# Kernel optimization log

Measured on AMD Instinct MI355X. Metric: run time of the kernel, lower is better.

## Reference

```python
import jax, jax.numpy as jnp
import numpy as np

N = 50000
E = 800000
NEG_SLOPE = 0.2
BN_EPS = 1e-5


def _gat_conv(x, src, dst, W, a_src, a_dst, bias, heads, out_ch, concat):
    # Linear projection per head: [N, heads, out_ch]
    h = (x @ W).reshape(-1, heads, out_ch)
    # Per-node attention terms alpha_src/alpha_dst: [N, heads]
    al_s = (h * a_src[None]).sum(-1)
    al_d = (h * a_dst[None]).sum(-1)
    # Edge logits with LeakyReLU: [E, heads]
    logits = jax.nn.leaky_relu(al_s[src] + al_d[dst], NEG_SLOPE)
    # Segment (scatter) softmax over edges grouped by destination node
    m = jax.ops.segment_max(logits, dst, num_segments=N)
    e = jnp.exp(logits - m[dst])
    s = jax.ops.segment_sum(e, dst, num_segments=N)
    alpha = e / (s[dst] + 1e-16)                      # [E, heads]
    # Weighted message aggregation: scatter-add to destinations
    msg = h[src] * alpha[:, :, None]                  # [E, heads, out_ch]
    out = jax.ops.segment_sum(msg, dst, num_segments=N)  # [N, heads, out_ch]
    out = out.reshape(-1, heads * out_ch) if concat else out.mean(axis=1)
    return out + bias


def _bn_eval(x, gamma, beta, mean, var):
    return (x - mean) * jax.lax.rsqrt(var + BN_EPS) * gamma + beta


def setup_inputs() -> dict:
    key = jax.random.key(0)
    ks = jax.random.split(key, 12)
    in_ch, hid, heads, out_cls = 128, 64, 2, 40
    return {
        "x": jax.random.normal(ks[0], (N, in_ch), jnp.float32),
        "edge_index": jax.random.randint(ks[1], (2, E), 0, N, jnp.int32),
        "W1": jax.random.normal(ks[2], (in_ch, heads * hid), jnp.float32) * 0.1,
        "a1_src": jax.random.normal(ks[3], (heads, hid), jnp.float32) * 0.1,
        "a1_dst": jax.random.normal(ks[4], (heads, hid), jnp.float32) * 0.1,
        "b1": jnp.zeros((heads * hid,), jnp.float32),
        "bn1_gamma": jnp.ones((heads * hid,), jnp.float32),
        "bn1_beta": jnp.zeros((heads * hid,), jnp.float32),
        "bn1_mean": jax.random.normal(ks[5], (heads * hid,), jnp.float32) * 0.1,
        "bn1_var": jax.random.uniform(ks[6], (heads * hid,), jnp.float32, 0.5, 1.5),
        "W2": jax.random.normal(ks[7], (heads * hid, out_cls), jnp.float32) * 0.1,
        "a2_src": jax.random.normal(ks[8], (1, out_cls), jnp.float32) * 0.1,
        "a2_dst": jax.random.normal(ks[9], (1, out_cls), jnp.float32) * 0.1,
        "b2": jnp.zeros((out_cls,), jnp.float32),
    }


def reference(x, edge_index, W1, a1_src, a1_dst, b1, bn1_gamma, bn1_beta,
              bn1_mean, bn1_var, W2, a2_src, a2_dst, b2):
    # add self loops
    loops = jnp.arange(N, dtype=edge_index.dtype)
    src = jnp.concatenate([edge_index[0], loops])
    dst = jnp.concatenate([edge_index[1], loops])
    # layer 1: GATConv(heads=2, concat) -> BN(eval) -> ReLU (dropout is eval no-op)
    h = _gat_conv(x, src, dst, W1, a1_src, a1_dst, b1, heads=2, out_ch=64, concat=True)
    h = jax.nn.relu(_bn_eval(h, bn1_gamma, bn1_beta, bn1_mean, bn1_var))
    # output layer: GATConv(heads=1, concat=False)
    out = _gat_conv(h, src, dst, W2, a2_src, a2_dst, b2, heads=1, out_ch=40, concat=False)
    return jax.nn.log_softmax(out, axis=1)
```

## Files before the change

### kernel.cpp

```cpp
#include <hip/hip_runtime.h>
#include <hip/hip_bf16.h>

#define NEG_SLOPE 0.2f
#define BN_EPS 1e-5f

#define NBLK 256
#define COARSE_SHIFT 9
#define COARSE_NPB 512

__device__ __forceinline__ float wred_sum(float v) {
    #pragma unroll
    for (int m = 32; m > 0; m >>= 1) v += __shfl_xor(v, m);
    return v;
}
__device__ __forceinline__ float wred_max(float v) {
    #pragma unroll
    for (int m = 32; m > 0; m >>= 1) v = fmaxf(v, __shfl_xor(v, m));
    return v;
}

__device__ __forceinline__ unsigned pack_bf16(float a, float b) {
    __hip_bfloat162 t;
    t.x = __float2bfloat16(a);
    t.y = __float2bfloat16(b);
    return *(unsigned*)&t;
}
__device__ __forceinline__ float2 unpack_bf16(unsigned u) {
    __hip_bfloat162 t = *(__hip_bfloat162*)&u;
    return {__bfloat162float(t.x), __bfloat162float(t.y)};
}

__device__ __forceinline__ unsigned enc_ord(float f) {
    unsigned u = __float_as_uint(f);
    return (u & 0x80000000u) ? ~u : (u | 0x80000000u);
}
__device__ __forceinline__ float dec_ord(unsigned e) {
    unsigned u = (e & 0x80000000u) ? (e ^ 0x80000000u) : ~e;
    return __uint_as_float(u);
}

__global__ __launch_bounds__(256) void part_hist(const int* __restrict__ ei, int E, int Et,
                                                 int chunk, int* __restrict__ hist, int nCoarse) {
    __shared__ int h[128];
    int b = blockIdx.x, t = threadIdx.x;
    if (t < 128) h[t] = 0;
    __syncthreads();
    int beg = b * chunk, end = min(beg + chunk, Et);
    for (int idx = beg + t; idx < end; idx += 256) {
        int d = (idx < E) ? ei[E + idx] : (idx - E);
        atomicAdd(&h[d >> COARSE_SHIFT], 1);
    }
    __syncthreads();
    if (t < nCoarse) hist[t * NBLK + b] = h[t];
}

__global__ __launch_bounds__(256) void coarse_total(const int* __restrict__ hist,
                                                    int* __restrict__ ctot) {
    __shared__ int red[256];
    int c = blockIdx.x, t = threadIdx.x;
    red[t] = hist[c * NBLK + t];
    __syncthreads();
    for (int off = 128; off > 0; off >>= 1) {
        if (t < off) red[t] += red[t + off];
        __syncthreads();
    }
    if (t == 0) ctot[c] = red[0];
}

__global__ __launch_bounds__(128) void coarse_scan(const int* __restrict__ ctot,
                                                   int* __restrict__ cbase, int nCoarse) {
    __shared__ int s[128];
    int t = threadIdx.x;
    int v = (t < nCoarse) ? ctot[t] : 0;
    s[t] = v;
    __syncthreads();
    for (int off = 1; off < 128; off <<= 1) {
        int u = (t >= off) ? s[t - off] : 0;
        __syncthreads();
        s[t] += u;
        __syncthreads();
    }
    if (t < nCoarse) cbase[t] = s[t] - v;
    if (t == 127) cbase[nCoarse] = s[127];
}

__global__ __launch_bounds__(64) void part_scan(int* __restrict__ hist,
                                                const int* __restrict__ cbase, int nCoarse) {
    int c = blockIdx.x, t = threadIdx.x;
    int base = cbase[c];
    int idx = c * NBLK + 4 * t;
    int4 v = *(int4*)&hist[idx];
    int sl = v.x + v.y + v.z + v.w;
    int inc = sl;
    #pragma unroll
    for (int off = 1; off < 64; off <<= 1) {
        int u = __shfl_up(inc, off);
        if (t >= off) inc += u;
    }
    int exc = inc - sl + base;
    int4 o;
    o.x = exc;
    o.y = exc + v.x;
    o.z = exc + v.x + v.y;
    o.w = exc + v.x + v.y + v.z;
    *(int4*)&hist[idx] = o;
}

__global__ __launch_bounds__(256) void part_scatter(const int* __restrict__ ei, int E, int Et,
                                                    int chunk, const int* __restrict__ hist,
                                                    unsigned* __restrict__ staged, int nCoarse) {
    __shared__ int cur[128];
    int b = blockIdx.x, t = threadIdx.x;
    if (t < nCoarse) cur[t] = hist[t * NBLK + b];
    __syncthreads();
    int beg = b * chunk, end = min(beg + chunk, Et);
    for (int idx = beg + t; idx < end; idx += 256) {
        int s, d;
        if (idx < E) { s = ei[idx]; d = ei[E + idx]; }
        else         { s = idx - E; d = idx - E; }
        int c = d >> COARSE_SHIFT;
        int pos = atomicAdd(&cur[c], 1);
        staged[pos] = ((unsigned)s << COARSE_SHIFT) | (unsigned)(d & (COARSE_NPB - 1));
    }
}

__global__ __launch_bounds__(512) void fine_place(const unsigned* __restrict__ staged,
                                                  const int* __restrict__ cbase,
                                                  int* __restrict__ offs,
                                                  int* __restrict__ csr, int Nn, int nCoarse) {
    __shared__ int hcnt[COARSE_NPB];
    __shared__ int scn[COARSE_NPB];
    int b = blockIdx.x, t = threadIdx.x;
    int node0 = b << COARSE_SHIFT;
    int nloc = min(COARSE_NPB, Nn - node0);
    hcnt[t] = 0;
    __syncthreads();
    int ebeg = cbase[b], eend = cbase[b + 1];
    for (int p = ebeg + t; p < eend; p += 512) {
        atomicAdd(&hcnt[staged[p] & (COARSE_NPB - 1)], 1);
    }
    __syncthreads();
    int val = hcnt[t];
    scn[t] = val;
    __syncthreads();
    for (int off = 1; off < COARSE_NPB; off <<= 1) {
        int u = (t >= off) ? scn[t - off] : 0;
        __syncthreads();
        scn[t] += u;
        __syncthreads();
    }
    int exc = ebeg + scn[t] - val;
    if (t < nloc) offs[node0 + t] = exc;
    if (b == nCoarse - 1 && t == 0) offs[Nn] = eend;
    hcnt[t] = exc;
    __syncthreads();
    for (int p = ebeg + t; p < eend; p += 512) {
        unsigned v = staged[p];
        int pos = atomicAdd(&hcnt[v & (COARSE_NPB - 1)], 1);
        csr[pos] = (int)(v >> COARSE_SHIFT);
    }
}

__global__ __launch_bounds__(256) void gemm1_tiled(const float* __restrict__ x,
                                                   const float* __restrict__ W,
                                                   const float* __restrict__ a1s,
                                                   const float* __restrict__ a1d,
                                                   unsigned* __restrict__ h1b,
                                                   float* __restrict__ als,
                                                   float* __restrict__ ald,
                                                   unsigned* __restrict__ gmax, int Nn) {
    __shared__ float As[64][33];
    __shared__ float Bs[32][132];
    __shared__ float4 red4[64][17];
    int t  = threadIdx.x;
    int tx = t & 15;
    int ty = t >> 4;
    int br = blockIdx.x * 64;

    float acc[4][8];
    #pragma unroll
    for (int i = 0; i < 4; ++i)
        #pragma unroll
        for (int j = 0; j < 8; ++j) acc[i][j] = 0.f;

    int k4  = t & 7;
    int rowA = t >> 3;

    for (int k0 = 0; k0 < 128; k0 += 32) {
        #pragma unroll
        for (int i = 0; i < 2; ++i) {
            int r  = rowA + 32 * i;
            int gr = min(br + r, Nn - 1);
            float4 v = *(const float4*)(x + (size_t)gr * 128 + k0 + 4 * k4);
            As[r][4 * k4 + 0] = v.x; As[r][4 * k4 + 1] = v.y;
            As[r][4 * k4 + 2] = v.z; As[r][4 * k4 + 3] = v.w;
        }
        #pragma unroll
        for (int i = 0; i < 4; ++i) {
            int f  = t + 256 * i;
            int kk = f >> 5, c4 = f & 31;
            *(float4*)&Bs[kk][4 * c4] = *(const float4*)(W + (size_t)(k0 + kk) * 128 + 4 * c4);
        }
        __syncthreads();
        #pragma unroll
        for (int kk = 0; kk < 32; ++kk) {
            float4 b0 = *(const float4*)&Bs[kk][4 * tx];
            float4 b1 = *(const float4*)&Bs[kk][64 + 4 * tx];
            #pragma unroll
            for (int i = 0; i < 4; ++i) {
                float a = As[4 * ty + i][kk];
                acc[i][0] += a * b0.x; acc[i][1] += a * b0.y;
                acc[i][2] += a * b0.z; acc[i][3] += a * b0.w;
                acc[i][4] += a * b1.x; acc[i][5] += a * b1.y;
                acc[i][6] += a * b1.z; acc[i][7] += a * b1.w;
            }
        }
        __syncthreads();
    }
    float s_lo[4], s_hi[4], d_lo[4], d_hi[4];
    #pragma unroll
    for (int j = 0; j < 4; ++j) {
        s_lo[j] = a1s[4 * tx + j];      s_hi[j] = a1s[64 + 4 * tx + j];
        d_lo[j] = a1d[4 * tx + j];      d_hi[j] = a1d[64 + 4 * tx + j];
    }
    #pragma unroll
    for (int i = 0; i < 4; ++i) {
        float4 pp = {0.f, 0.f, 0.f, 0.f};
        #pragma unroll
        for (int j = 0; j < 4; ++j) {
            pp.x += acc[i][j] * s_lo[j];
            pp.y += acc[i][4 + j] * s_hi[j];
            pp.z += acc[i][j] * d_lo[j];
            pp.w += acc[i][4 + j] * d_hi[j];
        }
        red4[4 * ty + i][tx] = pp;
        int r = br + 4 * ty + i;
        if (r < Nn) {
            uint2 lo = {pack_bf16(acc[i][0], acc[i][1]), pack_bf16(acc[i][2], acc[i][3])};
            uint2 hi = {pack_bf16(acc[i][4], acc[i][5]), pack_bf16(acc[i][6], acc[i][7])};
            *(uint2*)(h1b + (size_t)r * 64 + 2 * tx)      = lo;
            *(uint2*)(h1b + (size_t)r * 64 + 32 + 2 * tx) = hi;
        }
    }
    __syncthreads();
    if (t < 64) {
        int r = br + t;
        float4 s = {0.f, 0.f, 0.f, 0.f};
        #pragma unroll
        for (int xx = 0; xx < 16; ++xx) {
            float4 p = red4[t][xx];
            s.x += p.x; s.y += p.y; s.z += p.z; s.w += p.w;
        }
        if (r < Nn) {
            als[r * 2] = s.x; als[r * 2 + 1] = s.y;
            ald[r * 2] = s.z; ald[r * 2 + 1] = s.w;
        }
        float m0 = wred_max(s.x);
        float m1 = wred_max(s.y);
        if (t == 0) {
            atomicMax(&gmax[0], enc_ord(m0));
            atomicMax(&gmax[1], enc_ord(m1));
        }
    }
}

__global__ __launch_bounds__(256) void softagg1_kernel(const int* __restrict__ offs, const int* __restrict__ csr,
                            const unsigned* __restrict__ h1b,
                            const float* __restrict__ als, const float* __restrict__ ald,
                            const unsigned* __restrict__ gmax,
                            const float* __restrict__ b1, const float* __restrict__ gam,
                            const float* __restrict__ bet, const float* __restrict__ mean,
                            const float* __restrict__ var, float* __restrict__ hbn, int Nn) {
    int wid = threadIdx.x >> 6, lane = threadIdx.x & 63;
    int n = blockIdx.x * 4 + wid;
    if (n >= Nn) return;
    int b = offs[n], e = offs[n + 1];
    int sub = lane >> 4;
    int l16 = lane & 15;
    int head = l16 >> 3;
    float aldh = ald[n * 2 + head];
    float bound = dec_ord(gmax[head]) + aldh;
    bound = (bound > 0.f) ? bound : NEG_SLOPE * bound;

    float acc[8];
    #pragma unroll
    for (int j = 0; j < 8; ++j) acc[j] = 0.f;
    float den = 0.f;
    for (int p = b + sub; p < e; p += 4) {
        int s = csr[p];
        float al = als[s * 2 + head] + aldh;
        al = (al > 0.f) ? al : NEG_SLOPE * al;
        float ev = __expf(al - bound);
        uint4 v = *(const uint4*)(h1b + (size_t)s * 64 + 4 * l16);
        float2 f0 = unpack_bf16(v.x), f1 = unpack_bf16(v.y);
        float2 f2 = unpack_bf16(v.z), f3 = unpack_bf16(v.w);
        acc[0] += f0.x * ev; acc[1] += f0.y * ev;
        acc[2] += f1.x * ev; acc[3] += f1.y * ev;
        acc[4] += f2.x * ev; acc[5] += f2.y * ev;
        acc[6] += f3.x * ev; acc[7] += f3.y * ev;
        den += ev;
    }
    #pragma unroll
    for (int j = 0; j < 8; ++j) {
        acc[j] += __shfl_xor(acc[j], 16);
        acc[j] += __shfl_xor(acc[j], 32);
    }
    den += __shfl_xor(den, 16);
    den += __shfl_xor(den, 32);
    if (sub == 0) {
        float inv = 1.f / (den + 1e-16f);
        int c = 8 * l16;
        #pragma unroll
        for (int half = 0; half < 2; ++half) {
            int cc = c + 4 * half;
            float4 bb = *(const float4*)(b1 + cc);
            float4 gg = *(const float4*)(gam + cc);
            float4 be = *(const float4*)(bet + cc);
            float4 mm = *(const float4*)(mean + cc);
            float4 vv = *(const float4*)(var + cc);
            float4 o;
            o.x = fmaxf((acc[4*half+0] * inv + bb.x - mm.x) * rsqrtf(vv.x + BN_EPS) * gg.x + be.x, 0.f);
            o.y = fmaxf((acc[4*half+1] * inv + bb.y - mm.y) * rsqrtf(vv.y + BN_EPS) * gg.y + be.y, 0.f);
            o.z = fmaxf((acc[4*half+2] * inv + bb.z - mm.z) * rsqrtf(vv.z + BN_EPS) * gg.z + be.z, 0.f);
            o.w = fmaxf((acc[4*half+3] * inv + bb.w - mm.w) * rsqrtf(vv.w + BN_EPS) * gg.w + be.w, 0.f);
            *(float4*)(hbn + (size_t)n * 128 + cc) = o;
        }
    }
}

__global__ __launch_bounds__(256) void gemm2_tiled(const float* __restrict__ hbn,
                                                   const float* __restrict__ W2,
                                                   const float* __restrict__ a2s,
                                                   const float* __restrict__ a2d,
                                                   unsigned* __restrict__ h2b,
                                                   float* __restrict__ als, float* __restrict__ ald,
                                                   unsigned* __restrict__ gmax, int Nn) {
    __shared__ float As[64][33];
    __shared__ float Bs[128][68];
    __shared__ float redS[64][17];
    __shared__ float redD[64][17];
    int t  = threadIdx.x;
    int tx = t & 15;
    int ty = t >> 4;
    int br = blockIdx.x * 64;

    #pragma unroll
    for (int i = 0; i < 8; ++i) {
        int f  = t + 256 * i;
        int kk = f >> 4, c4 = f & 15;
        float4 v = {0.f, 0.f, 0.f, 0.f};
        if (c4 < 10) v = *(const float4*)(W2 + (size_t)kk * 40 + 4 * c4);
        *(float4*)&Bs[kk][4 * c4] = v;
    }
    float as4[4], ad4[4];
    #pragma unroll
    for (int j = 0; j < 4; ++j) {
        int c = 4 * tx + j;
        as4[j] = (c < 40) ? a2s[c] : 0.f;
        ad4[j] = (c < 40) ? a2d[c] : 0.f;
    }

    float acc[4][4];
    #pragma unroll
    for (int i = 0; i < 4; ++i)
        #pragma unroll
        for (int j = 0; j < 4; ++j) acc[i][j] = 0.f;

    int k4  = t & 7;
    int rowA = t >> 3;
    __syncthreads();

    for (int k0 = 0; k0 < 128; k0 += 32) {
        #pragma unroll
        for (int i = 0; i < 2; ++i) {
            int r  = rowA + 32 * i;
            int gr = min(br + r, Nn - 1);
            float4 v = *(const float4*)(hbn + (size_t)gr * 128 + k0 + 4 * k4);
            As[r][4 * k4 + 0] = v.x; As[r][4 * k4 + 1] = v.y;
            As[r][4 * k4 + 2] = v.z; As[r][4 * k4 + 3] = v.w;
        }
        __syncthreads();
        #pragma unroll
        for (int kk = 0; kk < 32; ++kk) {
            float4 b0 = *(const float4*)&Bs[k0 + kk][4 * tx];
            #pragma unroll
            for (int i = 0; i < 4; ++i) {
                float a = As[4 * ty + i][kk];
                acc[i][0] += a * b0.x; acc[i][1] += a * b0.y;
                acc[i][2] += a * b0.z; acc[i][3] += a * b0.w;
            }
        }
        __syncthreads();
    }
    #pragma unroll
    for (int i = 0; i < 4; ++i) {
        redS[4 * ty + i][tx] = acc[i][0] * as4[0] + acc[i][1] * as4[1] + acc[i][2] * as4[2] + acc[i][3] * as4[3];
        redD[4 * ty + i][tx] = acc[i][0] * ad4[0] + acc[i][1] * ad4[1] + acc[i][2] * ad4[2] + acc[i][3] * ad4[3];
        int r = br + 4 * ty + i;
        if (r < Nn) {
            uint2 pk = {pack_bf16(acc[i][0], acc[i][1]), pack_bf16(acc[i][2], acc[i][3])};
            *(uint2*)(h2b + (size_t)r * 32 + 2 * tx) = pk;
        }
    }
    __syncthreads();
    if (t < 64) {
        int r = br + t;
        float sS = 0.f, sD = 0.f;
        #pragma unroll
        for (int xx = 0; xx < 16; ++xx) { sS += redS[t][xx]; sD += redD[t][xx]; }
        if (r < Nn) { als[r] = sS; ald[r] = sD; }
        float m = wred_max(sS);
        if (t == 0) atomicMax(&gmax[2], enc_ord(m));
    }
}

__global__ __launch_bounds__(256) void softagg2_kernel(const int* __restrict__ offs, const int* __restrict__ csr,
                            const unsigned* __restrict__ h2b,
                            const float* __restrict__ als, const float* __restrict__ ald,
                            const unsigned* __restrict__ gmax,
                            const float* __restrict__ b2,
                            float* __restrict__ out, int Nn) {
    int wid = threadIdx.x >> 6, lane = threadIdx.x & 63;
    int n = blockIdx.x * 4 + wid;
    if (n >= Nn) return;
    int b = offs[n], e = offs[n + 1];
    float aldn = ald[n];
    float bound = dec_ord(gmax[2]) + aldn;
    bound = (bound > 0.f) ? bound : NEG_SLOPE * bound;

    int sub = lane >> 4;
    int l16 = lane & 15;
    float acc[4];
    #pragma unroll
    for (int j = 0; j < 4; ++j) acc[j] = 0.f;
    float den = 0.f;
    for (int p = b + sub; p < e; p += 4) {
        int s = csr[p];
        float l = als[s] + aldn;
        l = (l > 0.f) ? l : NEG_SLOPE * l;
        float ev = __expf(l - bound);
        uint2 v = *(const uint2*)(h2b + (size_t)s * 32 + 2 * l16);
        float2 f0 = unpack_bf16(v.x), f1 = unpack_bf16(v.y);
        acc[0] += f0.x * ev; acc[1] += f0.y * ev;
        acc[2] += f1.x * ev; acc[3] += f1.y * ev;
        den += ev;
    }
    #pragma unroll
    for (int j = 0; j < 4; ++j) {
        acc[j] += __shfl_xor(acc[j], 16);
        acc[j] += __shfl_xor(acc[j], 32);
    }
    den += __shfl_xor(den, 16);
    den += __shfl_xor(den, 32);
    float inv = 1.f / (den + 1e-16f);
    bool valid = (l16 < 10);
    float v0 = -1e30f, v1 = -1e30f, v2 = -1e30f, v3 = -1e30f;
    if (valid) {
        int c = 4 * l16;
        v0 = acc[0] * inv + b2[c];
        v1 = acc[1] * inv + b2[c + 1];
        v2 = acc[2] * inv + b2[c + 2];
        v3 = acc[3] * inv + b2[c + 3];
    }
    float m = wred_max(fmaxf(fmaxf(v0, v1), fmaxf(v2, v3)));
    float es = (valid && sub == 0)
             ? (__expf(v0 - m) + __expf(v1 - m) + __expf(v2 - m) + __expf(v3 - m)) : 0.f;
    float ssum = wred_sum(es);
    float lse = m + logf(ssum);
    if (sub == 0 && valid) {
        float4 o = {v0 - lse, v1 - lse, v2 - lse, v3 - lse};
        *(float4*)(out + (size_t)n * 40 + 4 * l16) = o;
    }
}

extern "C" void kernel_launch(void* const* d_in, const int* in_sizes, int n_in,
                              void* d_out, int out_size, void* d_ws, size_t ws_size,
                              hipStream_t stream) {
    const float* x    = (const float*)d_in[0];
    const int*   ei   = (const int*)d_in[1];
    const float* W1   = (const float*)d_in[2];
    const float* a1s  = (const float*)d_in[3];
    const float* a1d  = (const float*)d_in[4];
    const float* b1   = (const float*)d_in[5];
    const float* g1   = (const float*)d_in[6];
    const float* be1  = (const float*)d_in[7];
    const float* mn1  = (const float*)d_in[8];
    const float* vr1  = (const float*)d_in[9];
    const float* W2   = (const float*)d_in[10];
    const float* a2s  = (const float*)d_in[11];
    const float* a2d  = (const float*)d_in[12];
    const float* b2   = (const float*)d_in[13];
    float* out = (float*)d_out;

    const int N  = in_sizes[0] / 128;
    const int E  = in_sizes[1] / 2;
    const int Et = E + N;
    const int nCoarse = (N + COARSE_NPB - 1) >> COARSE_SHIFT;
    const int chunk   = (Et + NBLK - 1) / NBLK;

    char* p = (char*)d_ws;
    auto alloc = [&](size_t bytes) -> void* {
        void* r = (void*)p;
        p += (bytes + 255) & ~(size_t)255;
        return r;
    };
    int*      hist   = (int*)alloc((size_t)nCoarse * NBLK * 4);
    int*      ctot   = (int*)alloc((size_t)nCoarse * 4);
    int*      cbase  = (int*)alloc((size_t)(nCoarse + 1) * 4);
    int*      offs   = (int*)alloc((size_t)(N + 1) * 4);
    unsigned* staged = (unsigned*)alloc((size_t)Et * 4);
    int*      csr    = (int*)alloc((size_t)Et * 4);
    unsigned* h1b    = (unsigned*)alloc((size_t)N * 64 * 4);
    float*    al1sv  = (float*)alloc((size_t)N * 2 * 4);
    float*    al1dv  = (float*)alloc((size_t)N * 2 * 4);
    float*    hbn    = (float*)alloc((size_t)N * 128 * 4);
    unsigned* h2b    = (unsigned*)alloc((size_t)N * 32 * 4);
    float*    al2sv  = (float*)alloc((size_t)N * 4);
    float*    al2dv  = (float*)alloc((size_t)N * 4);
    unsigned* gmax   = (unsigned*)alloc(4 * 4);
    (void)ws_size;

    hipMemsetAsync(gmax, 0, 16, stream);

    part_hist<<<NBLK, 256, 0, stream>>>(ei, E, Et, chunk, hist, nCoarse);
    coarse_total<<<nCoarse, 256, 0, stream>>>(hist, ctot);
    coarse_scan<<<1, 128, 0, stream>>>(ctot, cbase, nCoarse);
    part_scan<<<nCoarse, 64, 0, stream>>>(hist, cbase, nCoarse);
    part_scatter<<<NBLK, 256, 0, stream>>>(ei, E, Et, chunk, hist, staged, nCoarse);
    fine_place<<<nCoarse, 512, 0, stream>>>(staged, cbase, offs, csr, N, nCoarse);

    gemm1_tiled<<<(N + 63) / 64, 256, 0, stream>>>(x, W1, a1s, a1d, h1b, al1sv, al1dv, gmax, N);
    softagg1_kernel<<<(N + 3) / 4, 256, 0, stream>>>(offs, csr, h1b, al1sv, al1dv, gmax,
                                                     b1, g1, be1, mn1, vr1, hbn, N);

    gemm2_tiled<<<(N + 63) / 64, 256, 0, stream>>>(hbn, W2, a2s, a2d, h2b, al2sv, al2dv, gmax, N);
    softagg2_kernel<<<(N + 3) / 4, 256, 0, stream>>>(offs, csr, h2b, al2sv, al2dv, gmax, b2, out, N);
}
```

Measured before the change: 277.2 us.

## Enlarge GEMM tiles to 128 rows with 8x8 register blocking and separate max kernels

```diff
diff --git a/kernel.cpp b/kernel.cpp
--- a/kernel.cpp
+++ b/kernel.cpp
@@ -16,6 +16,11 @@
 __device__ __forceinline__ float wred_max(float v) {
     #pragma unroll
     for (int m = 32; m > 0; m >>= 1) v = fmaxf(v, __shfl_xor(v, m));
+    return v;
+}
+__device__ __forceinline__ float xor16_sum(float v) {
+    #pragma unroll
+    for (int m = 1; m < 16; m <<= 1) v += __shfl_xor(v, m);
     return v;
 }
 
@@ -167,33 +172,31 @@
                                                    const float* __restrict__ a1d,
                                                    unsigned* __restrict__ h1b,
                                                    float* __restrict__ als,
-                                                   float* __restrict__ ald,
-                                                   unsigned* __restrict__ gmax, int Nn) {
-    __shared__ float As[64][33];
+                                                   float* __restrict__ ald, int Nn) {
+    __shared__ float Ast[32][132];
     __shared__ float Bs[32][132];
-    __shared__ float4 red4[64][17];
     int t  = threadIdx.x;
     int tx = t & 15;
     int ty = t >> 4;
-    int br = blockIdx.x * 64;
-
-    float acc[4][8];
-    #pragma unroll
-    for (int i = 0; i < 4; ++i)
+    int br = blockIdx.x * 128;
+
+    float acc[8][8];
+    #pragma unroll
+    for (int i = 0; i < 8; ++i)
         #pragma unroll
         for (int j = 0; j < 8; ++j) acc[i][j] = 0.f;
 
-    int k4  = t & 7;
+    int k4   = t & 7;
     int rowA = t >> 3;
 
     for (int k0 = 0; k0 < 128; k0 += 32) {
         #pragma unroll
-        for (int i = 0; i < 2; ++i) {
+        for (int i = 0; i < 4; ++i) {
             int r  = rowA + 32 * i;
             int gr = min(br + r, Nn - 1);
             float4 v = *(const float4*)(x + (size_t)gr * 128 + k0 + 4 * k4);
-            As[r][4 * k4 + 0] = v.x; As[r][4 * k4 + 1] = v.y;
-            As[r][4 * k4 + 2] = v.z; As[r][4 * k4 + 3] = v.w;
+            Ast[4 * k4 + 0][r] = v.x; Ast[4 * k4 + 1][r] = v.y;
+            Ast[4 * k4 + 2][r] = v.z; Ast[4 * k4 + 3][r] = v.w;
         }
         #pragma unroll
         for (int i = 0; i < 4; ++i) {
@@ -202,64 +205,78 @@
             *(float4*)&Bs[kk][4 * c4] = *(const float4*)(W + (size_t)(k0 + kk) * 128 + 4 * c4);
         }
         __syncthreads();
-        #pragma unroll
+        #pragma unroll 8
         for (int kk = 0; kk < 32; ++kk) {
-            float4 b0 = *(const float4*)&Bs[kk][4 * tx];
-            float4 b1 = *(const float4*)&Bs[kk][64 + 4 * tx];
+            float4 a0 = *(const float4*)&Ast[kk][8 * ty];
+            float4 a1 = *(const float4*)&Ast[kk][8 * ty + 4];
+            float4 b0 = *(const float4*)&Bs[kk][8 * tx];
+            float4 b1 = *(const float4*)&Bs[kk][8 * tx + 4];
+            float av[8] = {a0.x, a0.y, a0.z, a0.w, a1.x, a1.y, a1.z, a1.w};
+            float bv[8] = {b0.x, b0.y, b0.z, b0.w, b1.x, b1.y, b1.z, b1.w};
             #pragma unroll
-            for (int i = 0; i < 4; ++i) {
-                float a = As[4 * ty + i][kk];
-                acc[i][0] += a * b0.x; acc[i][1] += a * b0.y;
-                acc[i][2] += a * b0.z; acc[i][3] += a * b0.w;
-                acc[i][4] += a * b1.x; acc[i][5] += a * b1.y;
-                acc[i][6] += a * b1.z; acc[i][7] += a * b1.w;
-            }
-        }
-        __syncthreads();
-    }
-    float s_lo[4], s_hi[4], d_lo[4], d_hi[4];
-    #pragma unroll
-    for (int j = 0; j < 4; ++j) {
-        s_lo[j] = a1s[4 * tx + j];      s_hi[j] = a1s[64 + 4 * tx + j];
-        d_lo[j] = a1d[4 * tx + j];      d_hi[j] = a1d[64 + 4 * tx + j];
-    }
-    #pragma unroll
-    for (int i = 0; i < 4; ++i) {
-        float4 pp = {0.f, 0.f, 0.f, 0.f};
-        #pragma unroll
-        for (int j = 0; j < 4; ++j) {
-            pp.x += acc[i][j] * s_lo[j];
-            pp.y += acc[i][4 + j] * s_hi[j];
-            pp.z += acc[i][j] * d_lo[j];
-            pp.w += acc[i][4 + j] * d_hi[j];
-        }
-        red4[4 * ty + i][tx] = pp;
-        int r = br + 4 * ty + i;
+            for (int i = 0; i < 8; ++i)
+                #pragma unroll
+                for (int j = 0; j < 8; ++j) acc[i][j] += av[i] * bv[j];
+        }
+        __syncthreads();
+    }
+
+    float a_s[8], a_d[8];
+    #pragma unroll
+    for (int j = 0; j < 8; ++j) { a_s[j] = a1s[8 * tx + j]; a_d[j] = a1d[8 * tx + j]; }
+    bool h0 = (tx < 8);
+
+    #pragma unroll
+    for (int i = 0; i < 8; ++i) {
+        int r = br + 8 * ty + i;
         if (r < Nn) {
-            uint2 lo = {pack_bf16(acc[i][0], acc[i][1]), pack_bf16(acc[i][2], acc[i][3])};
-            uint2 hi = {pack_bf16(acc[i][4], acc[i][5]), pack_bf16(acc[i][6], acc[i][7])};
-            *(uint2*)(h1b + (size_t)r * 64 + 2 * tx)      = lo;
-            *(uint2*)(h1b + (size_t)r * 64 + 32 + 2 * tx) = hi;
-        }
-    }
-    __syncthreads();
-    if (t < 64) {
-        int r = br + t;
-        float4 s = {0.f, 0.f, 0.f, 0.f};
-        #pragma unroll
-        for (int xx = 0; xx < 16; ++xx) {
-            float4 p = red4[t][xx];
-            s.x += p.x; s.y += p.y; s.z += p.z; s.w += p.w;
-        }
-        if (r < Nn) {
-            als[r * 2] = s.x; als[r * 2 + 1] = s.y;
-            ald[r * 2] = s.z; ald[r * 2 + 1] = s.w;
-        }
-        float m0 = wred_max(s.x);
-        float m1 = wred_max(s.y);
-        if (t == 0) {
-            atomicMax(&gmax[0], enc_ord(m0));
-            atomicMax(&gmax[1], enc_ord(m1));
+            uint4 pk;
+            pk.x = pack_bf16(acc[i][0], acc[i][1]);
+            pk.y = pack_bf16(acc[i][2], acc[i][3]);
+            pk.z = pack_bf16(acc[i][4], acc[i][5]);
+            pk.w = pack_bf16(acc[i][6], acc[i][7]);
+            *(uint4*)(h1b + (size_t)r * 64 + 4 * tx) = pk;
+        }
+        float ps = 0.f, pd = 0.f;
+        #pragma unroll
+        for (int j = 0; j < 8; ++j) { ps += acc[i][j] * a_s[j]; pd += acc[i][j] * a_d[j]; }
+        float s0 = xor16_sum(h0 ? ps : 0.f);
+        float s1 = xor16_sum(h0 ? 0.f : ps);
+        float d0 = xor16_sum(h0 ? pd : 0.f);
+        float d1 = xor16_sum(h0 ? 0.f : pd);
+        if (tx == 0 && r < Nn) {
+            als[r * 2] = s0; als[r * 2 + 1] = s1;
+            ald[r * 2] = d0; ald[r * 2 + 1] = d1;
+        }
+    }
+}
+
+template <int H>
+__global__ __launch_bounds__(256) void almax_kernel(const float* __restrict__ als,
+                                                    unsigned* __restrict__ gmax,
+                                                    int off, int Nn) {
+    __shared__ float red[4][H];
+    int t = threadIdx.x;
+    float m[H];
+    #pragma unroll
+    for (int h = 0; h < H; ++h) m[h] = -1e30f;
+    for (int n = blockIdx.x * 256 + t; n < Nn; n += gridDim.x * 256) {
+        #pragma unroll
+        for (int h = 0; h < H; ++h) m[h] = fmaxf(m[h], als[n * H + h]);
+    }
+    #pragma unroll
+    for (int h = 0; h < H; ++h) m[h] = wred_max(m[h]);
+    int wid = t >> 6;
+    if ((t & 63) == 0) {
+        #pragma unroll
+        for (int h = 0; h < H; ++h) red[wid][h] = m[h];
+    }
+    __syncthreads();
+    if (t == 0) {
+        #pragma unroll
+        for (int h = 0; h < H; ++h) {
+            float mm = fmaxf(fmaxf(red[0][h], red[1][h]), fmaxf(red[2][h], red[3][h]));
+            atomicMax(&gmax[off + h], enc_ord(mm));
         }
     }
 }
@@ -334,24 +351,14 @@
                                                    const float* __restrict__ a2d,
                                                    unsigned* __restrict__ h2b,
                                                    float* __restrict__ als, float* __restrict__ ald,
-                                                   unsigned* __restrict__ gmax, int Nn) {
-    __shared__ float As[64][33];
-    __shared__ float Bs[128][68];
-    __shared__ float redS[64][17];
-    __shared__ float redD[64][17];
+                                                   int Nn) {
+    __shared__ float Ast[32][132];
+    __shared__ float Bs[32][68];
     int t  = threadIdx.x;
     int tx = t & 15;
     int ty = t >> 4;
-    int br = blockIdx.x * 64;
-
-    #pragma unroll
-    for (int i = 0; i < 8; ++i) {
-        int f  = t + 256 * i;
-        int kk = f >> 4, c4 = f & 15;
-        float4 v = {0.f, 0.f, 0.f, 0.f};
-        if (c4 < 10) v = *(const float4*)(W2 + (size_t)kk * 40 + 4 * c4);
-        *(float4*)&Bs[kk][4 * c4] = v;
-    }
+    int br = blockIdx.x * 128;
+
     float as4[4], ad4[4];
     #pragma unroll
     for (int j = 0; j < 4; ++j) {
@@ -360,57 +367,60 @@
         ad4[j] = (c < 40) ? a2d[c] : 0.f;
     }
 
-    float acc[4][4];
-    #pragma unroll
-    for (int i = 0; i < 4; ++i)
+    float acc[8][4];
+    #pragma unroll
+    for (int i = 0; i < 8; ++i)
         #pragma unroll
         for (int j = 0; j < 4; ++j) acc[i][j] = 0.f;
 
-    int k4  = t & 7;
+    int k4   = t & 7;
     int rowA = t >> 3;
-    __syncthreads();
 
     for (int k0 = 0; k0 < 128; k0 += 32) {
         #pragma unroll
-        for (int i = 0; i < 2; ++i) {
+        for (int i = 0; i < 4; ++i) {
             int r  = rowA + 32 * i;
             int gr = min(br + r, Nn - 1);
             float4 v = *(const float4*)(hbn + (size_t)gr * 128 + k0 + 4 * k4);
-            As[r][4 * k4 + 0] = v.x; As[r][4 * k4 + 1] = v.y;
-            As[r][4 * k4 + 2] = v.z; As[r][4 * k4 + 3] = v.w;
-        }
-        __syncthreads();
-        #pragma unroll
+            Ast[4 * k4 + 0][r] = v.x; Ast[4 * k4 + 1][r] = v.y;
+            Ast[4 * k4 + 2][r] = v.z; Ast[4 * k4 + 3][r] = v.w;
+        }
+        #pragma unroll
+        for (int i = 0; i < 2; ++i) {
+            int f  = t + 256 * i;
+            int kk = f >> 4, c4 = f & 15;
+            float4 v = {0.f, 0.f, 0.f, 0.f};
+            if (c4 < 10) v = *(const float4*)(W2 + (size_t)(k0 + kk) * 40 + 4 * c4);
+            *(float4*)&Bs[kk][4 * c4] = v;
+        }
+        __syncthreads();
+        #pragma unroll 8
         for (int kk = 0; kk < 32; ++kk) {
-            float4 b0 = *(const float4*)&Bs[k0 + kk][4 * tx];
+            float4 a0 = *(const float4*)&Ast[kk][8 * ty];
+            float4 a1 = *(const float4*)&Ast[kk][8 * ty + 4];
+            float4 b0 = *(const float4*)&Bs[kk][4 * tx];
+            float av[8] = {a0.x, a0.y, a0.z, a0.w, a1.x, a1.y, a1.z, a1.w};
             #pragma unroll
-            for (int i = 0; i < 4; ++i) {
-                float a = As[4 * ty + i][kk];
-                acc[i][0] += a * b0.x; acc[i][1] += a * b0.y;
-                acc[i][2] += a * b0.z; acc[i][3] += a * b0.w;
+            for (int i = 0; i < 8; ++i) {
+                acc[i][0] += av[i] * b0.x; acc[i][1] += av[i] * b0.y;
+                acc[i][2] += av[i] * b0.z; acc[i][3] += av[i] * b0.w;
             }
         }
         __syncthreads();
     }
-    #pragma unroll
-    for (int i = 0; i < 4; ++i) {
-        redS[4 * ty + i][tx] = acc[i][0] * as4[0] + acc[i][1] * as4[1] + acc[i][2] * as4[2] + acc[i][3] * as4[3];
-        redD[4 * ty + i][tx] = acc[i][0] * ad4[0] + acc[i][1] * ad4[1] + acc[i][2] * ad4[2] + acc[i][3] * ad4[3];
-        int r = br + 4 * ty + i;
+
+    #pragma unroll
+    for (int i = 0; i < 8; ++i) {
+        int r = br + 8 * ty + i;
         if (r < Nn) {
             uint2 pk = {pack_bf16(acc[i][0], acc[i][1]), pack_bf16(acc[i][2], acc[i][3])};
             *(uint2*)(h2b + (size_t)r * 32 + 2 * tx) = pk;
         }
-    }
-    __syncthreads();
-    if (t < 64) {
-        int r = br + t;
-        float sS = 0.f, sD = 0.f;
-        #pragma unroll
-        for (int xx = 0; xx < 16; ++xx) { sS += redS[t][xx]; sD += redD[t][xx]; }
-        if (r < Nn) { als[r] = sS; ald[r] = sD; }
-        float m = wred_max(sS);
-        if (t == 0) atomicMax(&gmax[2], enc_ord(m));
+        float ps = acc[i][0] * as4[0] + acc[i][1] * as4[1] + acc[i][2] * as4[2] + acc[i][3] * as4[3];
+        float pd = acc[i][0] * ad4[0] + acc[i][1] * ad4[1] + acc[i][2] * ad4[2] + acc[i][3] * ad4[3];
+        float sS = xor16_sum(ps);
+        float sD = xor16_sum(pd);
+        if (tx == 0 && r < Nn) { als[r] = sS; ald[r] = sD; }
     }
 }
 
@@ -529,10 +539,12 @@
     part_scatter<<<NBLK, 256, 0, stream>>>(ei, E, Et, chunk, hist, staged, nCoarse);
     fine_place<<<nCoarse, 512, 0, stream>>>(staged, cbase, offs, csr, N, nCoarse);
 
-    gemm1_tiled<<<(N + 63) / 64, 256, 0, stream>>>(x, W1, a1s, a1d, h1b, al1sv, al1dv, gmax, N);
+    gemm1_tiled<<<(N + 127) / 128, 256, 0, stream>>>(x, W1, a1s, a1d, h1b, al1sv, al1dv, N);
+    almax_kernel<2><<<64, 256, 0, stream>>>(al1sv, gmax, 0, N);
     softagg1_kernel<<<(N + 3) / 4, 256, 0, stream>>>(offs, csr, h1b, al1sv, al1dv, gmax,
                                                      b1, g1, be1, mn1, vr1, hbn, N);
 
-    gemm2_tiled<<<(N + 63) / 64, 256, 0, stream>>>(hbn, W2, a2s, a2d, h2b, al2sv, al2dv, gmax, N);
+    gemm2_tiled<<<(N + 127) / 128, 256, 0, stream>>>(hbn, W2, a2s, a2d, h2b, al2sv, al2dv, N);
+    almax_kernel<1><<<64, 256, 0, stream>>>(al2sv, gmax, 2, N);
     softagg2_kernel<<<(N + 3) / 4, 256, 0, stream>>>(offs, csr, h2b, al2sv, al2dv, gmax, b2, out, N);
 }
```

Result: faster. 267.6 us (-3.4%).
